# Performance work log

Hardware: AMD Instinct MI355X
Metric: run time of the kernel (lower is better)

## Reference

```python
import jax, jax.numpy as jnp
import numpy as np

ANCHORS = np.array([[10,13],[16,30],[33,23],[30,61],[62,45],[59,119],[116,90],[156,198],[373,326]], np.float32)
ANCHOR_MASK = [[6, 7, 8], [3, 4, 5], [0, 1, 2]]
INPUT_SHAPE = np.array([416, 416], np.float32)  # (h, w)
NUM_CLASSES = 80
EPS = 1e-7


def _bce(pred, target):
    # clip_by_tensor + binary cross entropy, as in the torch module
    p = jnp.clip(pred, EPS, 1.0 - EPS)
    return -target * jnp.log(p) - (1.0 - target) * jnp.log(1.0 - p)


def _box_iou(b1, b2):
    # b1: (..., 1, 4), b2: (..., n, 4), center-format xywh (normalized)
    b1_xy, b1_wh = b1[..., :2], b1[..., 2:4]
    b2_xy, b2_wh = b2[..., :2], b2[..., 2:4]
    b1_min, b1_max = b1_xy - b1_wh / 2.0, b1_xy + b1_wh / 2.0
    b2_min, b2_max = b2_xy - b2_wh / 2.0, b2_xy + b2_wh / 2.0
    inter_wh = jnp.maximum(jnp.minimum(b1_max, b2_max) - jnp.maximum(b1_min, b2_min), 0.0)
    inter = inter_wh[..., 0] * inter_wh[..., 1]
    a1 = b1_wh[..., 0] * b1_wh[..., 1]
    a2 = b2_wh[..., 0] * b2_wh[..., 1]
    return inter / (a1 + a2 - inter)


def _decode(y_pred, anchors):
    # y_pred: (b, 3*(5+C), h, w) -> raw: (b, 3, h, w, 5+C)
    b, _, h, w = y_pred.shape
    raw = y_pred.reshape(b, 3, 5 + NUM_CLASSES, h, w).transpose(0, 1, 3, 4, 2)
    gy, gx = jnp.meshgrid(jnp.arange(h, dtype=y_pred.dtype), jnp.arange(w, dtype=y_pred.dtype), indexing='ij')
    grid_xy = jnp.stack([gx, gy], axis=-1)  # (h, w, 2)
    pred_xy = jax.nn.sigmoid(raw[..., 0:2])
    pred_wh = raw[..., 2:4]                 # raw tw, th (MSE'd against log target)
    pred_conf = jax.nn.sigmoid(raw[..., 4:5])
    pred_class = jax.nn.sigmoid(raw[..., 5:])
    # decoded, normalized boxes for IoU-based negative mining
    box_xy = (pred_xy + grid_xy) / jnp.array([w, h], y_pred.dtype)
    box_wh = jnp.exp(pred_wh) * anchors.reshape(3, 1, 1, 2) / jnp.asarray(INPUT_SHAPE[::-1].copy())
    pred_box = jnp.concatenate([box_xy, box_wh], axis=-1)  # (b,3,h,w,4)
    return grid_xy, pred_box, pred_xy, pred_wh, pred_conf, pred_class


def _layer_loss(y_pred, y_true, target, anchors):
    b, _, h, w = y_pred.shape
    grid_xy, pred_box, pred_xy, pred_wh, pred_conf, pred_class = _decode(y_pred, anchors)
    object_mask = y_true[..., 4:5]
    true_xy = y_true[..., 0:2] * jnp.array([h, w], y_pred.dtype) - grid_xy
    true_wh = jnp.log(y_true[..., 2:4] * jnp.asarray(INPUT_SHAPE[::-1].copy()) / anchors.reshape(3, 1, 1, 2))
    true_wh = jnp.where(object_mask > 0, true_wh, jnp.zeros_like(true_wh))
    loss_scale = 2.0 - y_true[..., 2:3] * y_true[..., 3:4]
    # negative mask: every grid/anchor prediction vs all true boxes of its image (vectorized over batch)
    iou = _box_iou(pred_box[:, :, :, :, None, :], target[:, None, None, None, :, :4])  # (b,3,h,w,n)
    best_iou = jnp.max(iou, axis=-1)
    neg = (best_iou < 0.5).astype(y_pred.dtype)[..., None]
    neg_mask = (1.0 - object_mask) * neg
    loss_xy = jnp.sum(object_mask * loss_scale * _bce(pred_xy, true_xy))
    loss_wh = jnp.sum(object_mask * loss_scale * 0.5 * (pred_wh - true_wh) ** 2)
    conf_bce = _bce(pred_conf, object_mask)
    loss_conf = jnp.sum(object_mask * conf_bce) + jnp.sum(neg_mask * conf_bce)
    loss_cls = jnp.sum(object_mask * _bce(pred_class, y_true[..., 5:]))
    return loss_xy + loss_wh + loss_conf + loss_cls


def setup_inputs() -> dict:
    key = jax.random.key(0)
    ks = jax.random.split(key, 7)
    grids = [13, 26, 52]
    b, n = 32, 20
    inp = {}
    for i, g in enumerate(grids):
        inp[f'y_pred{i}'] = jax.random.normal(ks[i], (b, 3 * (5 + NUM_CLASSES), g, g), jnp.float32)
        # y_true values in (0.05, 0.95): keeps log(true_wh) and 1/y_true grads bounded
        inp[f'y_true{i}'] = 0.05 + 0.9 * jax.random.uniform(ks[3 + i], (b, 3, g, g, 5 + NUM_CLASSES), jnp.float32)
    inp['target'] = 0.05 + 0.9 * jax.random.uniform(ks[6], (b, n, 5), jnp.float32)
    return inp


def reference(y_pred0, y_pred1, y_pred2, y_true0, y_true1, y_true2, target):
    total = jnp.zeros((), jnp.float32)
    for yp, yt, mask in ((y_pred0, y_true0, ANCHOR_MASK[0]),
                         (y_pred1, y_true1, ANCHOR_MASK[1]),
                         (y_pred2, y_true2, ANCHOR_MASK[2])):
        total = total + _layer_loss(yp, yt, target, jnp.asarray(ANCHORS[mask]))
    return total
```

## Files before the change

### kernel.cpp

```cpp
#include <hip/hip_runtime.h>
#include <math.h>

#define BLOCK 256
#define NB0 64
#define NB1 254
#define NB2 1014
#define NBLOCKS (NB0 + NB1 + NB2)

typedef float f4 __attribute__((ext_vector_type(4)));

__constant__ float c_anch[9][2] = {
    {116.f, 90.f}, {156.f, 198.f}, {373.f, 326.f},
    { 30.f, 61.f}, { 62.f,  45.f}, { 59.f, 119.f},
    { 10.f, 13.f}, { 16.f,  30.f}, { 33.f,  23.f}
};

__device__ __forceinline__ float softplusf(float x) {
    float ax = fabsf(x);
    return fmaxf(x, 0.f) + __logf(1.f + __expf(-ax));
}

__device__ __forceinline__ float sigmoidf(float x) {
    return __fdividef(1.f, 1.f + __expf(-x));
}

__global__ __launch_bounds__(BLOCK) void yolo_loss_main(
    const float* __restrict__ p0, const float* __restrict__ p1, const float* __restrict__ p2,
    const float* __restrict__ t0, const float* __restrict__ t1, const float* __restrict__ t2,
    const float* __restrict__ tgt, float* __restrict__ out)
{
    int blk = blockIdx.x;
    const float* pred;
    const float* tru;
    int layer, g, cells, bbase;
    if (blk < NB0)            { layer = 0; pred = p0; tru = t0; g = 13; cells = 16224;  bbase = 0; }
    else if (blk < NB0 + NB1) { layer = 1; pred = p1; tru = t1; g = 26; cells = 64896;  bbase = NB0; }
    else                      { layer = 2; pred = p2; tru = t2; g = 52; cells = 259584; bbase = NB0 + NB1; }

    int idx = (blk - bbase) * BLOCK + threadIdx.x;
    float acc = 0.f;

    if (idx < cells) {
        int hw = g * g;
        int ij = idx % hw;
        int a  = (idx / hw) % 3;
        int b  = idx / (3 * hw);
        int i  = ij / g;
        int j  = ij - i * g;

        const float* pb = pred + (size_t)((b * 3 + a) * 85) * hw + ij;
        const float* tb = tru + (size_t)((b * 3 + a) * hw + ij) * 85;

        float r0 = pb[0];
        float r1 = pb[hw];
        float r2 = pb[2 * hw];
        float r3 = pb[3 * hw];
        float r4 = pb[4 * hw];

        f4 y = *reinterpret_cast<const f4*>(tb);
        float y0 = y.x, y1 = y.y, y2 = y.z, y3 = y.w;
        float mask = tb[4];

        float gf = (float)g, gx = (float)j, gy = (float)i;
        float aw = c_anch[layer * 3 + a][0];
        float ah = c_anch[layer * 3 + a][1];

        float true_x = y0 * gf - gx;
        float true_y = y1 * gf - gy;
        float ls = 2.f - y2 * y3;
        float lxy = (softplusf(r0) - true_x * r0) + (softplusf(r1) - true_y * r1);
        acc += mask * ls * lxy;

        float tw = __logf(y2 * (416.f / aw));
        float th = __logf(y3 * (416.f / ah));
        float dw = r2 - tw, dh = r3 - th;
        acc += mask * ls * 0.5f * (dw * dw + dh * dh);

        float cbce = softplusf(r4) - mask * r4;

        float sx = sigmoidf(r0);
        float sy = sigmoidf(r1);
        float bx = __fdividef(sx + gx, gf);
        float by = __fdividef(sy + gy, gf);
        float bw = __expf(r2) * aw * (1.f / 416.f);
        float bh = __expf(r3) * ah * (1.f / 416.f);
        float a1 = bw * bh;
        float b1minx = bx - 0.5f * bw, b1maxx = bx + 0.5f * bw;
        float b1miny = by - 0.5f * bh, b1maxy = by + 0.5f * bh;

        const float* tg = tgt + b * 20 * 5;
        float best = 0.f;
#pragma unroll 4
        for (int k = 0; k < 20; k++) {
            float tx  = tg[k * 5 + 0];
            float ty  = tg[k * 5 + 1];
            float tww = tg[k * 5 + 2];
            float thh = tg[k * 5 + 3];
            float iw = fminf(b1maxx, tx + 0.5f * tww) - fmaxf(b1minx, tx - 0.5f * tww);
            float ih = fminf(b1maxy, ty + 0.5f * thh) - fmaxf(b1miny, ty - 0.5f * thh);
            iw = fmaxf(iw, 0.f);
            ih = fmaxf(ih, 0.f);
            float inter = iw * ih;
            float iou = __fdividef(inter, a1 + tww * thh - inter);
            best = fmaxf(best, iou);
        }
        float neg = (best < 0.5f) ? 1.f : 0.f;
        acc += mask * cbce + (1.f - mask) * neg * cbce;

        const f4* t4 = reinterpret_cast<const f4*>(tb + 5);
        float c0 = 0.f, c1 = 0.f, c2 = 0.f, c3 = 0.f;
#pragma unroll 5
        for (int k = 0; k < 20; k++) {
            f4 t = t4[k];
            const float* px = pb + (5 + 4 * k) * hw;
            float x0 = px[0];
            float x1 = px[hw];
            float x2 = px[2 * hw];
            float x3 = px[3 * hw];
            c0 += softplusf(x0) - t.x * x0;
            c1 += softplusf(x1) - t.y * x1;
            c2 += softplusf(x2) - t.z * x2;
            c3 += softplusf(x3) - t.w * x3;
        }
        acc += mask * ((c0 + c1) + (c2 + c3));
    }

    for (int off = 32; off > 0; off >>= 1)
        acc += __shfl_down(acc, off, 64);
    __shared__ float sh[BLOCK / 64];
    if ((threadIdx.x & 63) == 0)
        sh[threadIdx.x >> 6] = acc;
    __syncthreads();
    if (threadIdx.x == 0) {
        float s = 0.f;
        for (int wv = 0; wv < BLOCK / 64; wv++) s += sh[wv];
        atomicAdd(out, s);
    }
}

extern "C" void kernel_launch(void* const* d_in, const int* in_sizes, int n_in,
                              void* d_out, int out_size, void* d_ws, size_t ws_size,
                              hipStream_t stream) {
    const float* p0  = (const float*)d_in[0];
    const float* t0  = (const float*)d_in[1];
    const float* p1  = (const float*)d_in[2];
    const float* t1  = (const float*)d_in[3];
    const float* p2  = (const float*)d_in[4];
    const float* t2  = (const float*)d_in[5];
    const float* tgt = (const float*)d_in[6];

    hipMemsetAsync(d_out, 0, sizeof(float), stream);
    yolo_loss_main<<<NBLOCKS, BLOCK, 0, stream>>>(p0, p1, p2, t0, t1, t2, tgt, (float*)d_out);
}
```

Baseline: 294.4 us.

## Stage y_true through LDS with coalesced loads and a transpose

The y_true rows (85 floats per cell, cell-major) were read per thread with a stride of 85 floats, so lanes' accesses were poorly coalesced. The kernel now has the block cooperatively load 16-column chunks of its 256 contiguous rows into a padded shared-memory tile, which each thread then reads for its own cell. This adds several __syncthreads barriers and about 16 KB of LDS per block, which may reduce occupancy.

```diff
diff --git a/kernel.cpp b/kernel.cpp
--- a/kernel.cpp
+++ b/kernel.cpp
@@ -6,8 +6,6 @@
 #define NB1 254
 #define NB2 1014
 #define NBLOCKS (NB0 + NB1 + NB2)
-
-typedef float f4 __attribute__((ext_vector_type(4)));
 
 __constant__ float c_anch[9][2] = {
     {116.f, 90.f}, {156.f, 198.f}, {373.f, 326.f},
@@ -37,19 +35,48 @@
     else if (blk < NB0 + NB1) { layer = 1; pred = p1; tru = t1; g = 26; cells = 64896;  bbase = NB0; }
     else                      { layer = 2; pred = p2; tru = t2; g = 52; cells = 259584; bbase = NB0 + NB1; }
 
-    int idx = (blk - bbase) * BLOCK + threadIdx.x;
-    float acc = 0.f;
-
-    if (idx < cells) {
-        int hw = g * g;
+    const int tid = threadIdx.x;
+    const int cellbase = (blk - bbase) * BLOCK;
+    const int idx = cellbase + tid;
+    const bool valid = idx < cells;
+
+    __shared__ float lds[16][BLOCK + 1];
+
+    const int hw = g * g;
+    const float* pb = pred;
+    float aw = 1.f, ah = 1.f, gx = 0.f, gy = 0.f;
+    int b = 0;
+    if (valid) {
         int ij = idx % hw;
         int a  = (idx / hw) % 3;
-        int b  = idx / (3 * hw);
+        b      = idx / (3 * hw);
         int i  = ij / g;
         int j  = ij - i * g;
-
-        const float* pb = pred + (size_t)((b * 3 + a) * 85) * hw + ij;
-        const float* tb = tru + (size_t)((b * 3 + a) * hw + ij) * 85;
+        pb = pred + (size_t)((b * 3 + a) * 85) * hw + ij;
+        aw = c_anch[layer * 3 + a][0];
+        ah = c_anch[layer * 3 + a][1];
+        gx = (float)j; gy = (float)i;
+    }
+    const float gf = (float)g;
+
+    float acc = 0.f;
+    float cls = 0.f;
+    float mask = 0.f;
+
+    const float* src0 = tru + (size_t)cellbase * 85;
+
+#pragma unroll
+    for (int k = 0; k < 16; k++) {
+        int e = k * BLOCK + tid;
+        int cl = e >> 4, c = e & 15;
+        if (cellbase + cl < cells)
+            lds[c][cl] = src0[(size_t)cl * 85 + c];
+    }
+    __syncthreads();
+
+    if (valid) {
+        float y0 = lds[0][tid], y1 = lds[1][tid], y2 = lds[2][tid], y3 = lds[3][tid];
+        mask = lds[4][tid];
 
         float r0 = pb[0];
         float r1 = pb[hw];
@@ -57,14 +84,6 @@
         float r3 = pb[3 * hw];
         float r4 = pb[4 * hw];
 
-        f4 y = *reinterpret_cast<const f4*>(tb);
-        float y0 = y.x, y1 = y.y, y2 = y.z, y3 = y.w;
-        float mask = tb[4];
-
-        float gf = (float)g, gx = (float)j, gy = (float)i;
-        float aw = c_anch[layer * 3 + a][0];
-        float ah = c_anch[layer * 3 + a][1];
-
         float true_x = y0 * gf - gx;
         float true_y = y1 * gf - gy;
         float ls = 2.f - y2 * y3;
@@ -77,7 +96,6 @@
         acc += mask * ls * 0.5f * (dw * dw + dh * dh);
 
         float cbce = softplusf(r4) - mask * r4;
-
         float sx = sigmoidf(r0);
         float sy = sigmoidf(r1);
         float bx = __fdividef(sx + gx, gf);
@@ -107,31 +125,65 @@
         float neg = (best < 0.5f) ? 1.f : 0.f;
         acc += mask * cbce + (1.f - mask) * neg * cbce;
 
-        const f4* t4 = reinterpret_cast<const f4*>(tb + 5);
-        float c0 = 0.f, c1 = 0.f, c2 = 0.f, c3 = 0.f;
-#pragma unroll 5
-        for (int k = 0; k < 20; k++) {
-            f4 t = t4[k];
-            const float* px = pb + (5 + 4 * k) * hw;
-            float x0 = px[0];
-            float x1 = px[hw];
-            float x2 = px[2 * hw];
-            float x3 = px[3 * hw];
-            c0 += softplusf(x0) - t.x * x0;
-            c1 += softplusf(x1) - t.y * x1;
-            c2 += softplusf(x2) - t.z * x2;
-            c3 += softplusf(x3) - t.w * x3;
-        }
-        acc += mask * ((c0 + c1) + (c2 + c3));
-    }
+#pragma unroll
+        for (int c = 5; c < 16; c++) {
+            float x = pb[c * hw];
+            float t = lds[c][tid];
+            cls += softplusf(x) - t * x;
+        }
+    }
+    __syncthreads();
+
+    for (int c0 = 16; c0 < 80; c0 += 16) {
+        const float* src = src0 + c0;
+#pragma unroll
+        for (int k = 0; k < 16; k++) {
+            int e = k * BLOCK + tid;
+            int cl = e >> 4, c = e & 15;
+            if (cellbase + cl < cells)
+                lds[c][cl] = src[(size_t)cl * 85 + c];
+        }
+        __syncthreads();
+        if (valid) {
+#pragma unroll
+            for (int c = 0; c < 16; c++) {
+                float x = pb[(c0 + c) * hw];
+                float t = lds[c][tid];
+                cls += softplusf(x) - t * x;
+            }
+        }
+        __syncthreads();
+    }
+
+    {
+        const float* src = src0 + 80;
+#pragma unroll
+        for (int k = 0; k < 5; k++) {
+            int e = k * BLOCK + tid;
+            int cl = e / 5, c = e - cl * 5;
+            if (cellbase + cl < cells)
+                lds[c][cl] = src[(size_t)cl * 85 + c];
+        }
+        __syncthreads();
+        if (valid) {
+#pragma unroll
+            for (int c = 0; c < 5; c++) {
+                float x = pb[(80 + c) * hw];
+                float t = lds[c][tid];
+                cls += softplusf(x) - t * x;
+            }
+        }
+    }
+
+    if (valid) acc += mask * cls;
 
     for (int off = 32; off > 0; off >>= 1)
         acc += __shfl_down(acc, off, 64);
     __shared__ float sh[BLOCK / 64];
-    if ((threadIdx.x & 63) == 0)
-        sh[threadIdx.x >> 6] = acc;
+    if ((tid & 63) == 0)
+        sh[tid >> 6] = acc;
     __syncthreads();
-    if (threadIdx.x == 0) {
+    if (tid == 0) {
         float s = 0.f;
         for (int wv = 0; wv < BLOCK / 64; wv++) s += sh[wv];
         atomicAdd(out, s);
```

Measured after the change: 300.1 us. Within noise of the previous version (+1.9%).
